# Performance work log

Hardware: AMD Instinct MI355X
Metric: run time of the kernel (lower is better)

The kernel has to match this reference:

```python
import jax, jax.numpy as jnp
import numpy as np

BN_EPS = 1e-5
TEMPERATURE = 256 ** 0.5  # sqrt(c2), since cv3 = ScaledDotProductAttention(c2)


def conv_bn_silu(x, w, gamma, beta, mean, var):
    # Conv2d(k=3, s=1, pad='same', bias=False) -> BatchNorm2d (running stats) -> SiLU
    y = jax.lax.conv_general_dilated(
        x, w, window_strides=(1, 1), padding='SAME',
        dimension_numbers=('NCHW', 'OIHW', 'NCHW'))
    scale = (gamma / jnp.sqrt(var + BN_EPS))[None, :, None, None]
    shift = (beta - mean * gamma / jnp.sqrt(var + BN_EPS))[None, :, None, None]
    y = y * scale + shift
    return y * jax.nn.sigmoid(y)  # SiLU


def setup_inputs() -> dict:
    key = jax.random.key(0)
    ks = jax.random.split(key, 8)
    B, C, H, W = 16, 256, 64, 64
    Ch = 128  # hidden channels c_ = int(c2 * e)
    x = jax.random.normal(ks[0], (B, C, H, W), dtype=jnp.float32)
    w1 = jax.random.normal(ks[1], (Ch, C, 3, 3), dtype=jnp.float32) * 0.05
    g1 = jnp.ones((Ch,), jnp.float32) + 0.1 * jax.random.normal(ks[2], (Ch,), dtype=jnp.float32)
    b1 = 0.1 * jax.random.normal(ks[3], (Ch,), dtype=jnp.float32)
    m1 = 0.1 * jax.random.normal(ks[4], (Ch,), dtype=jnp.float32)
    v1 = jnp.ones((Ch,), jnp.float32) + 0.5 * jax.random.uniform(ks[5], (Ch,), dtype=jnp.float32)
    w2 = jax.random.normal(ks[6], (C, Ch, 3, 3), dtype=jnp.float32) * 0.05
    g2 = jnp.ones((C,), jnp.float32)
    b2 = jnp.zeros((C,), jnp.float32)
    m2 = 0.1 * jax.random.normal(ks[7], (C,), dtype=jnp.float32)
    v2 = jnp.ones((C,), jnp.float32) + 0.5 * jax.random.uniform(jax.random.fold_in(key, 99), (C,), dtype=jnp.float32)
    return {"x": x, "w1": w1, "g1": g1, "b1": b1, "m1": m1, "v1": v1,
            "w2": w2, "g2": g2, "b2": b2, "m2": m2, "v2": v2}


def reference(x, w1, g1, b1, m1, v1, w2, g2, b2, m2, v2):
    y = conv_bn_silu(x, w1, g1, b1, m1, v1)       # [B, 128, H, W]
    y = conv_bn_silu(y, w2, g2, b2, m2, v2)       # [B, 256, H, W]
    B, C, H, W = y.shape
    q = y.reshape(B, C, H * W)                    # q = k^T = v, all views of y
    # channel-channel attention: scores [B, C, C]
    scores = jnp.einsum('bcn,bdn->bcd', q / TEMPERATURE, q)
    attn = jax.nn.softmax(scores, axis=-1)        # dropout is identity in eval
    out = jnp.einsum('bcd,bdn->bcn', attn, q).reshape(B, C, H, W)
    return x + out  # shortcut: c1 == c2
```

## Files before the change

kernel.cpp:

```cpp
#include <hip/hip_runtime.h>
#include <math.h>

#define BB 16
#define C1 256
#define CHD 128
#define NN 4096
#define INV_T (1.0f/16.0f)

typedef _Float16 half8 __attribute__((ext_vector_type(8)));
typedef __attribute__((ext_vector_type(4))) float f32x4;

__device__ inline unsigned short f2h(float f) {
    _Float16 h = (_Float16)f;
    return __builtin_bit_cast(unsigned short, h);
}

#define GLDS(g, l) __builtin_amdgcn_global_load_lds(                              \
    (const __attribute__((address_space(1))) unsigned int*)(g),                   \
    (__attribute__((address_space(3))) unsigned int*)(l), 16, 0, 0)

__global__ __launch_bounds__(256) void nchw_to_nhwc_f16(
    const float* __restrict__ x, unsigned short* __restrict__ xh, int C)
{
    const int c0 = blockIdx.x * 64;
    const int hp = blockIdx.y;
    const int b  = blockIdx.z;

    if (hp == 0 || hp == 65) {
        for (int idx = threadIdx.x; idx < 1024; idx += 256) {
            int w = idx >> 4, cq = (idx & 15) * 4;
            ushort4 z; z.x = z.y = z.z = z.w = 0;
            *(ushort4*)&xh[(((size_t)b * 66 + hp) * 64 + w) * C + c0 + cq] = z;
        }
        return;
    }
    const int h = hp - 1;
    __shared__ float ts[64][65];
    for (int idx = threadIdx.x; idx < 4096; idx += 256) {
        int cl = idx >> 6, w = idx & 63;
        ts[cl][w] = x[(((size_t)b * C + c0 + cl) * 64 + h) * 64 + w];
    }
    __syncthreads();
    for (int idx = threadIdx.x; idx < 1024; idx += 256) {
        int w = idx >> 4, cq = (idx & 15) * 4;
        ushort4 o;
        o.x = f2h(ts[cq + 0][w]); o.y = f2h(ts[cq + 1][w]);
        o.z = f2h(ts[cq + 2][w]); o.w = f2h(ts[cq + 3][w]);
        *(ushort4*)&xh[(((size_t)b * 66 + hp) * 64 + w) * C + c0 + cq] = o;
    }
}

__global__ __launch_bounds__(256) void pack_w_kernel(
    const float* __restrict__ w, unsigned short* __restrict__ wT, int Cout, int Cin)
{
    int idx = blockIdx.x * 256 + threadIdx.x;
    int total = Cout * Cin * 9;
    if (idx >= total) return;
    int ci = idx % Cin; int t = idx / Cin; int co = t % Cout; int kk = t / Cout;
    wT[idx] = f2h(w[((size_t)co * Cin + ci) * 9 + kk]);
}

__global__ __launch_bounds__(256) void zero_y1h_pads(unsigned short* __restrict__ y1h)
{
    int idx = blockIdx.x * 256 + threadIdx.x;
    int b = idx >> 12;
    int row = ((idx >> 11) & 1) ? 65 : 0;
    int inner = idx & 2047;
    ushort4 z; z.x = z.y = z.z = z.w = 0;
    *(ushort4*)&y1h[(((size_t)b * 66 + row) * 64) * 128 + inner * 4] = z;
}

__global__ __launch_bounds__(256) void conv_mfma_kernel(
    const unsigned short* __restrict__ xh, const unsigned short* __restrict__ wT,
    const float* __restrict__ gamma, const float* __restrict__ beta,
    const float* __restrict__ mean, const float* __restrict__ var,
    unsigned short* __restrict__ outNHWC,
    unsigned short* __restrict__ yhi, unsigned short* __restrict__ yhiT,
    int Cin, int Cout)
{
    const int tid  = threadIdx.x;
    const int wid  = tid >> 6;
    const int lane = tid & 63;
    const int ln   = lane & 15;
    const int q    = lane >> 4;
    const int coBase = blockIdx.x * 64;
    const int h0     = blockIdx.y * 4;
    const int b      = blockIdx.z;

    __shared__ unsigned short xs[6 * 66 * 32];
    __shared__ unsigned short ws[9 * 64 * 32];
    __shared__ float bnsc[64], bnsh[64];

    if (tid < 64) {
        int co = coBase + tid;
        float sc = gamma[co] * rsqrtf(var[co] + 1e-5f);
        bnsc[tid] = sc;
        bnsh[tid] = beta[co] - mean[co] * sc;
    }
    if (tid < 48) {
        int r = tid >> 3, cpart = tid & 7;
        int col = (cpart < 4) ? 0 : 65;
        ushort4 z; z.x = z.y = z.z = z.w = 0;
        *(ushort4*)&xs[r * 2112 + col * 32 + (cpart & 3) * 8] = z;
        *(ushort4*)&xs[r * 2112 + col * 32 + (cpart & 3) * 8 + 4] = z;
    }
    __syncthreads();

    f32x4 acc[4][4] = {};

    const int nChunk = Cin >> 5;
    for (int ck = 0; ck < nChunk; ck++) {
        const int ci0 = ck << 5;
        for (int it = wid; it < 60; it += 4) {
            if (it < 36) {
                int el   = it * 512 + lane * 8;
                int kkco = el >> 5;
                int kk   = kkco >> 6;
                int co   = kkco & 63;
                int cip  = el & 31;
                const unsigned short* g =
                    wT + (((size_t)kk * Cout + coBase + co) * Cin + ci0 + cip);
                GLDS(g, ws + it * 512);
            } else {
                int j = it - 36;
                int r = j >> 2, p = j & 3;
                int w   = p * 16 + (lane >> 2);
                int cip = (lane & 3) * 8;
                const unsigned short* g =
                    xh + ((((size_t)b * 66 + h0 + r) * 64 + w) * Cin + ci0 + cip);
                GLDS(g, xs + r * 2112 + (1 + p * 16) * 32);
            }
        }
        __syncthreads();

#pragma unroll
        for (int kk = 0; kk < 9; kk++) {
            const int kh = kk / 3, kw = kk % 3;
            half8 af[4], bfr[4];
#pragma unroll
            for (int mi = 0; mi < 4; mi++)
                af[mi] = *(const half8*)&ws[(kk * 64 + mi * 16 + ln) * 32 + q * 8];
#pragma unroll
            for (int ni = 0; ni < 4; ni++)
                bfr[ni] = *(const half8*)&xs[(wid + kh) * 2112 + (ni * 16 + ln + kw) * 32 + q * 8];
#pragma unroll
            for (int mi = 0; mi < 4; mi++)
#pragma unroll
                for (int ni = 0; ni < 4; ni++)
                    acc[mi][ni] = __builtin_amdgcn_mfma_f32_16x16x32_f16(
                        af[mi], bfr[ni], acc[mi][ni], 0, 0, 0);
        }
        __syncthreads();
    }

    const int orow = h0 + wid;
    if (outNHWC) {
#pragma unroll
        for (int mi = 0; mi < 4; mi++) {
            int col0 = mi * 16 + q * 4;
            float s0 = bnsc[col0 + 0], h0s = bnsh[col0 + 0];
            float s1 = bnsc[col0 + 1], h1s = bnsh[col0 + 1];
            float s2 = bnsc[col0 + 2], h2s = bnsh[col0 + 2];
            float s3 = bnsc[col0 + 3], h3s = bnsh[col0 + 3];
#pragma unroll
            for (int ni = 0; ni < 4; ni++) {
                int w = ni * 16 + ln;
                f32x4 a = acc[mi][ni];
                float t0 = a.x * s0 + h0s, t1 = a.y * s1 + h1s;
                float t2 = a.z * s2 + h2s, t3 = a.w * s3 + h3s;
                ushort4 o;
                o.x = f2h(t0 / (1.f + __expf(-t0)));
                o.y = f2h(t1 / (1.f + __expf(-t1)));
                o.z = f2h(t2 / (1.f + __expf(-t2)));
                o.w = f2h(t3 / (1.f + __expf(-t3)));
                *(ushort4*)&outNHWC[(((size_t)b * 66 + orow + 1) * 64 + w) * Cout
                                    + coBase + col0] = o;
            }
        }
    } else {
#pragma unroll
        for (int mi = 0; mi < 4; mi++) {
            int col0 = mi * 16 + q * 4;
#pragma unroll
            for (int ni = 0; ni < 4; ni++) {
                int w = ni * 16 + ln;
                f32x4 a = acc[mi][ni];
                float vals[4] = {a.x, a.y, a.z, a.w};
                ushort4 hv;
                unsigned short* hvp = (unsigned short*)&hv;
#pragma unroll
                for (int r = 0; r < 4; r++) {
                    int co = coBase + col0 + r;
                    float t = vals[r] * bnsc[col0 + r] + bnsh[col0 + r];
                    float s = t / (1.f + __expf(-t));
                    hvp[r] = f2h(s);
                    yhi[(((size_t)b * Cout + co) * 64 + orow) * 64 + w] = hvp[r];
                }
                *(ushort4*)&yhiT[((size_t)b * 4096 + orow * 64 + w) * Cout
                                 + coBase + col0] = hv;
            }
        }
    }
}

__global__ __launch_bounds__(256) void scores_mfma_kernel(
    const unsigned short* __restrict__ yhi, float* __restrict__ scores)
{
    static const int TI[10] = {0,0,0,0,1,1,1,2,2,3};
    static const int TJ[10] = {0,1,2,3,1,2,3,2,3,3};
    const int b  = blockIdx.z;
    const int ti = TI[blockIdx.x], tj = TJ[blockIdx.x];
    const int cB = ti * 64;
    const int dB = tj * 64;
    const int tid  = threadIdx.x;
    const int wid  = tid >> 6;
    const int lane = tid & 63;
    const int ln   = lane & 15;
    const int q    = lane >> 4;
    const int wm   = wid >> 1, wn = wid & 1;

    __shared__ unsigned short As[64 * 128];
    __shared__ unsigned short Bs[64 * 128];

    const int rl = lane >> 4;
    const int gl = lane & 15;

    f32x4 acc[2][2] = {};

    for (int ck = 0; ck < 32; ck++) {
        const int n0 = ck * 128;
        for (int it = wid; it < 32; it += 4) {
            const int tile = it >> 4;
            const int j = it & 15;
            const int r = j * 4 + rl;
            const int gq = gl ^ (r & 7);
            const int rowAbs = (tile ? dB : cB) + r;
            const unsigned short* g =
                yhi + ((size_t)b * 256 + rowAbs) * 4096 + n0 + gq * 8;
            GLDS(g, (tile ? Bs : As) + j * 512);
        }
        __syncthreads();

#pragma unroll
        for (int kwin = 0; kwin < 4; kwin++) {
            half8 ah[2], bh[2];
#pragma unroll
            for (int mi = 0; mi < 2; mi++) {
                int row = wm * 32 + mi * 16 + ln;
                ah[mi] = *(const half8*)&As[row * 128 + ((kwin * 4 + q) ^ (ln & 7)) * 8];
            }
#pragma unroll
            for (int ni = 0; ni < 2; ni++) {
                int row = wn * 32 + ni * 16 + ln;
                bh[ni] = *(const half8*)&Bs[row * 128 + ((kwin * 4 + q) ^ (ln & 7)) * 8];
            }
#pragma unroll
            for (int mi = 0; mi < 2; mi++)
#pragma unroll
                for (int ni = 0; ni < 2; ni++)
                    acc[mi][ni] = __builtin_amdgcn_mfma_f32_16x16x32_f16(
                        ah[mi], bh[ni], acc[mi][ni], 0, 0, 0);
        }
        __syncthreads();
    }

#pragma unroll
    for (int mi = 0; mi < 2; mi++)
#pragma unroll
        for (int ni = 0; ni < 2; ni++) {
            f32x4 a = acc[mi][ni];
            float vals[4];
            vals[0] = a.x * INV_T; vals[1] = a.y * INV_T;
            vals[2] = a.z * INV_T; vals[3] = a.w * INV_T;
            int c0 = cB + wm * 32 + mi * 16 + q * 4;
            int d  = dB + wn * 32 + ni * 16 + ln;
#pragma unroll
            for (int r = 0; r < 4; r++)
                scores[((size_t)b * C1 + c0 + r) * C1 + d] = vals[r];
            if (ti != tj) {
                float4 tv = {vals[0], vals[1], vals[2], vals[3]};
                *(float4*)&scores[((size_t)b * C1 + d) * C1 + c0] = tv;
            }
        }
}

__global__ __launch_bounds__(64) void softmax_kernel(
    const float* __restrict__ scores, unsigned short* __restrict__ attn16)
{
    const int row = blockIdx.x;
    const float* p = scores + (size_t)row * C1;
    const int lane = threadIdx.x;

    float4 v = ((const float4*)p)[lane];
    float m = fmaxf(fmaxf(v.x, v.y), fmaxf(v.z, v.w));
#pragma unroll
    for (int off = 32; off >= 1; off >>= 1)
        m = fmaxf(m, __shfl_xor(m, off, 64));

    float4 e;
    e.x = expf(v.x - m); e.y = expf(v.y - m);
    e.z = expf(v.z - m); e.w = expf(v.w - m);
    float s = e.x + e.y + e.z + e.w;
#pragma unroll
    for (int off = 32; off >= 1; off >>= 1)
        s += __shfl_xor(s, off, 64);
    float inv = 1.f / s;
    ushort4 o;
    o.x = f2h(e.x * inv); o.y = f2h(e.y * inv);
    o.z = f2h(e.z * inv); o.w = f2h(e.w * inv);
    *(ushort4*)&attn16[(size_t)row * C1 + lane * 4] = o;
}

__global__ __launch_bounds__(256) void out_mfma_kernel(
    const unsigned short* __restrict__ attn16, const unsigned short* __restrict__ yhiT,
    const float* __restrict__ x, float* __restrict__ out)
{
    const int b  = blockIdx.z;
    const int cB = blockIdx.y * 64;
    const int nB = blockIdx.x * 128;
    const int tid  = threadIdx.x;
    const int wid  = tid >> 6;
    const int lane = tid & 63;
    const int ln   = lane & 15;
    const int q    = lane >> 4;
    const int wm   = wid >> 1, wn = wid & 1;

    __shared__ unsigned short As[64 * 64];
    __shared__ unsigned short Bs[128 * 64];

    const int r8 = lane >> 3;
    const int gq = (lane & 7) ^ r8;

    f32x4 acc[2][4] = {};

    for (int ck = 0; ck < 4; ck++) {
        const int d0 = ck * 64;
        for (int it = wid; it < 24; it += 4) {
            if (it < 8) {
                const unsigned short* g =
                    attn16 + ((size_t)b * 256 + cB + it * 8 + r8) * 256 + d0 + gq * 8;
                GLDS(g, As + it * 512);
            } else {
                int j = it - 8;
                const unsigned short* g =
                    yhiT + ((size_t)b * 4096 + nB + j * 8 + r8) * 256 + d0 + gq * 8;
                GLDS(g, Bs + j * 512);
            }
        }
        __syncthreads();

#pragma unroll
        for (int kwin = 0; kwin < 2; kwin++) {
            const int cc = (((kwin * 4 + q) ^ (ln & 7))) * 8;
            half8 af[2], bfr[4];
#pragma unroll
            for (int mi = 0; mi < 2; mi++)
                af[mi] = *(const half8*)&As[(wm * 32 + mi * 16 + ln) * 64 + cc];
#pragma unroll
            for (int ni = 0; ni < 4; ni++)
                bfr[ni] = *(const half8*)&Bs[(wn * 64 + ni * 16 + ln) * 64 + cc];
#pragma unroll
            for (int mi = 0; mi < 2; mi++)
#pragma unroll
                for (int ni = 0; ni < 4; ni++)
                    acc[mi][ni] = __builtin_amdgcn_mfma_f32_16x16x32_f16(
                        af[mi], bfr[ni], acc[mi][ni], 0, 0, 0);
        }
        __syncthreads();
    }

#pragma unroll
    for (int mi = 0; mi < 2; mi++)
#pragma unroll
        for (int ni = 0; ni < 4; ni++) {
            f32x4 a = acc[mi][ni];
            float vals[4] = {a.x, a.y, a.z, a.w};
#pragma unroll
            for (int r = 0; r < 4; r++) {
                int c = cB + wm * 32 + mi * 16 + q * 4 + r;
                int n = nB + wn * 64 + ni * 16 + ln;
                size_t o = ((size_t)b * C1 + c) * NN + n;
                out[o] = x[o] + vals[r];
            }
        }
}

extern "C" void kernel_launch(void* const* d_in, const int* in_sizes, int n_in,
                              void* d_out, int out_size, void* d_ws, size_t ws_size,
                              hipStream_t stream)
{
    const float* x  = (const float*)d_in[0];
    const float* w1 = (const float*)d_in[1];
    const float* g1 = (const float*)d_in[2];
    const float* b1 = (const float*)d_in[3];
    const float* m1 = (const float*)d_in[4];
    const float* v1 = (const float*)d_in[5];
    const float* w2 = (const float*)d_in[6];
    const float* g2 = (const float*)d_in[7];
    const float* b2 = (const float*)d_in[8];
    const float* m2 = (const float*)d_in[9];
    const float* v2 = (const float*)d_in[10];
    float* out = (float*)d_out;

    unsigned short* xh   = (unsigned short*)d_ws;
    unsigned short* y1h  = xh  + (size_t)17301504;
    unsigned short* wt1  = y1h + (size_t)8650752;
    unsigned short* wt2  = wt1 + (size_t)294912;
    unsigned short* yhiT = wt2 + (size_t)294912;
    unsigned short* yhi  = xh;
    float*          sc   = (float*)y1h;
    unsigned short* attn16 = (unsigned short*)(sc + 1048576);

    nchw_to_nhwc_f16<<<dim3(C1 / 64, 66, BB), 256, 0, stream>>>(x, xh, C1);
    pack_w_kernel<<<(9 * CHD * C1 + 255) / 256, 256, 0, stream>>>(w1, wt1, CHD, C1);
    pack_w_kernel<<<(9 * C1 * CHD + 255) / 256, 256, 0, stream>>>(w2, wt2, C1, CHD);
    zero_y1h_pads<<<256, 256, 0, stream>>>(y1h);

    conv_mfma_kernel<<<dim3(CHD / 64, 16, BB), 256, 0, stream>>>(
        xh, wt1, g1, b1, m1, v1, y1h, nullptr, nullptr, C1, CHD);
    conv_mfma_kernel<<<dim3(C1 / 64, 16, BB), 256, 0, stream>>>(
        y1h, wt2, g2, b2, m2, v2, nullptr, yhi, yhiT, CHD, C1);

    scores_mfma_kernel<<<dim3(10, 1, BB), 256, 0, stream>>>(yhi, sc);
    softmax_kernel<<<dim3(BB * C1), 64, 0, stream>>>(sc, attn16);
    out_mfma_kernel<<<dim3(NN / 128, 4, BB), 256, 0, stream>>>(attn16, yhiT, x, out);
}
```

Baseline: 332.5 us.

## Swizzle conv LDS tiles and use 8-row tiles for second conv

Applies an XOR swizzle to the 16-byte chunks that global_load_lds writes into the weight and input LDS tiles, and applies the matching swizzle to the MFMA fragment reads. The goal is to remove LDS bank conflicts when fragments are read. The conv kernel is also templated on the number of waves, and the second conv now uses 8 waves covering 8 output rows per block. Each weight tile is then reused across more rows, at the cost of more LDS per block and fewer blocks.

```diff
diff --git a/kernel.cpp b/kernel.cpp
--- a/kernel.cpp
+++ b/kernel.cpp
@@ -70,7 +70,8 @@
     *(ushort4*)&y1h[(((size_t)b * 66 + row) * 64) * 128 + inner * 4] = z;
 }
 
-__global__ __launch_bounds__(256) void conv_mfma_kernel(
+template<int NW>
+__global__ __launch_bounds__(NW * 64) void conv_mfma_kernel(
     const unsigned short* __restrict__ xh, const unsigned short* __restrict__ wT,
     const float* __restrict__ gamma, const float* __restrict__ beta,
     const float* __restrict__ mean, const float* __restrict__ var,
@@ -84,10 +85,10 @@
     const int ln   = lane & 15;
     const int q    = lane >> 4;
     const int coBase = blockIdx.x * 64;
-    const int h0     = blockIdx.y * 4;
+    const int h0     = blockIdx.y * NW;
     const int b      = blockIdx.z;
 
-    __shared__ unsigned short xs[6 * 66 * 32];
+    __shared__ unsigned short xs[(NW + 2) * 66 * 32];
     __shared__ unsigned short ws[9 * 64 * 32];
     __shared__ float bnsc[64], bnsh[64];
 
@@ -97,7 +98,7 @@
         bnsc[tid] = sc;
         bnsh[tid] = beta[co] - mean[co] * sc;
     }
-    if (tid < 48) {
+    if (tid < (NW + 2) * 8) {
         int r = tid >> 3, cpart = tid & 7;
         int col = (cpart < 4) ? 0 : 65;
         ushort4 z; z.x = z.y = z.z = z.w = 0;
@@ -108,26 +109,26 @@
 
     f32x4 acc[4][4] = {};
 
+    const int swz = (((lane & 3) ^ ((lane >> 3) & 3))) * 8;
+    const int nIssue = 36 + (NW + 2) * 4;
+
     const int nChunk = Cin >> 5;
     for (int ck = 0; ck < nChunk; ck++) {
         const int ci0 = ck << 5;
-        for (int it = wid; it < 60; it += 4) {
+        for (int it = wid; it < nIssue; it += NW) {
             if (it < 36) {
-                int el   = it * 512 + lane * 8;
-                int kkco = el >> 5;
+                int kkco = it * 16 + (lane >> 2);
                 int kk   = kkco >> 6;
                 int co   = kkco & 63;
-                int cip  = el & 31;
                 const unsigned short* g =
-                    wT + (((size_t)kk * Cout + coBase + co) * Cin + ci0 + cip);
+                    wT + (((size_t)kk * Cout + coBase + co) * Cin + ci0 + swz);
                 GLDS(g, ws + it * 512);
             } else {
                 int j = it - 36;
                 int r = j >> 2, p = j & 3;
-                int w   = p * 16 + (lane >> 2);
-                int cip = (lane & 3) * 8;
+                int w = p * 16 + (lane >> 2);
                 const unsigned short* g =
-                    xh + ((((size_t)b * 66 + h0 + r) * 64 + w) * Cin + ci0 + cip);
+                    xh + ((((size_t)b * 66 + h0 + r) * 64 + w) * Cin + ci0 + swz);
                 GLDS(g, xs + r * 2112 + (1 + p * 16) * 32);
             }
         }
@@ -137,12 +138,14 @@
         for (int kk = 0; kk < 9; kk++) {
             const int kh = kk / 3, kw = kk % 3;
             half8 af[4], bfr[4];
+            const int sw = (q ^ ((ln >> 1) & 3)) * 8;
+            const int sx = (q ^ (((ln + kw + 63) >> 1) & 3)) * 8;
 #pragma unroll
             for (int mi = 0; mi < 4; mi++)
-                af[mi] = *(const half8*)&ws[(kk * 64 + mi * 16 + ln) * 32 + q * 8];
+                af[mi] = *(const half8*)&ws[(kk * 64 + mi * 16 + ln) * 32 + sw];
 #pragma unroll
             for (int ni = 0; ni < 4; ni++)
-                bfr[ni] = *(const half8*)&xs[(wid + kh) * 2112 + (ni * 16 + ln + kw) * 32 + q * 8];
+                bfr[ni] = *(const half8*)&xs[(wid + kh) * 2112 + (ni * 16 + ln + kw) * 32 + sx];
 #pragma unroll
             for (int mi = 0; mi < 4; mi++)
 #pragma unroll
@@ -416,9 +419,9 @@
     pack_w_kernel<<<(9 * C1 * CHD + 255) / 256, 256, 0, stream>>>(w2, wt2, C1, CHD);
     zero_y1h_pads<<<256, 256, 0, stream>>>(y1h);
 
-    conv_mfma_kernel<<<dim3(CHD / 64, 16, BB), 256, 0, stream>>>(
+    conv_mfma_kernel<4><<<dim3(CHD / 64, 16, BB), 256, 0, stream>>>(
         xh, wt1, g1, b1, m1, v1, y1h, nullptr, nullptr, C1, CHD);
-    conv_mfma_kernel<<<dim3(C1 / 64, 16, BB), 256, 0, stream>>>(
+    conv_mfma_kernel<8><<<dim3(C1 / 64, 8, BB), 512, 0, stream>>>(
         y1h, wt2, g2, b2, m2, v2, nullptr, yhi, yhiT, CHD, C1);
 
     scores_mfma_kernel<<<dim3(10, 1, BB), 256, 0, stream>>>(yhi, sc);
```

Result: no change. 335.2 us (+0.8%).
